# Performance work log

Hardware: AMD Instinct MI355X
Metric: run time of the kernel (lower is better)

Reference implementation:

```python
import jax, jax.numpy as jnp
import numpy as np

N_TOK = 16384   # total tokens (batch*seq)
H = 2048        # hidden_size
I = 768         # moe_intermediate_size (per-expert MLP width)
TOPK = 8        # num_experts_per_tok


def setup_inputs() -> dict:
    key = jax.random.key(0)
    ks = jax.random.split(key, 7)
    hidden_states = jax.random.normal(ks[0], (N_TOK, H), dtype=jnp.float32)
    # expert_mask[j, k] != 0 means token k selected this expert at top-k slot j
    expert_mask = jax.random.randint(ks[1], (TOPK, N_TOK), 0, 2, dtype=jnp.int32)
    routing_weights = jax.random.uniform(ks[2], (N_TOK, TOPK), dtype=jnp.float32)
    final_hidden_states = jax.random.normal(ks[3], (N_TOK, H), dtype=jnp.float32)
    gate_w = jax.random.normal(ks[4], (I, H), dtype=jnp.float32) * 0.02
    up_w = jax.random.normal(ks[5], (I, H), dtype=jnp.float32) * 0.02
    down_w = jax.random.normal(ks[6], (H, I), dtype=jnp.float32) * 0.02
    return {
        "hidden_states": hidden_states,
        "expert_mask": expert_mask,
        "routing_weights": routing_weights,
        "final_hidden_states": final_hidden_states,
        "gate_w": gate_w,
        "up_w": up_w,
        "down_w": down_w,
    }


def reference(hidden_states, expert_mask, routing_weights, final_hidden_states,
              gate_w, up_w, down_w):
    # forward_expert: gather selected tokens, SwiGLU MLP, scale by routing weight,
    # scatter-add into final_hidden_states. Equivalent jit-friendly form: the
    # combined routing weight per token is w[k] = sum_j mask[j,k]*routing_weights[k,j]
    # (tokens selected multiple times are summed, matching index_add_ semantics),
    # and unselected tokens get w[k]=0 so they contribute nothing.
    g = hidden_states @ gate_w.T                       # [N, I]
    u = hidden_states @ up_w.T                         # [N, I]
    y = (jax.nn.silu(g) * u) @ down_w.T                # [N, H]
    w = jnp.einsum('jk,kj->k', expert_mask.astype(y.dtype), routing_weights)  # [N]
    return final_hidden_states + y * w[:, None]
```

## Files before the change

kernel.cpp:

```cpp
#include <hip/hip_runtime.h>
#include <stdint.h>

#define NTOK 16384
#define HD   2048
#define ID   768
#define TOPK 8

typedef __bf16 bf16x8 __attribute__((ext_vector_type(8)));
typedef float  floatx4 __attribute__((ext_vector_type(4)));
typedef unsigned short ushort8 __attribute__((ext_vector_type(8)));

__device__ __forceinline__ unsigned short f32_to_bf16_rne(float f) {
    union { float f; uint32_t u; } v; v.f = f;
    uint32_t u = v.u;
    u += 0x7FFFu + ((u >> 16) & 1u);
    return (unsigned short)(u >> 16);
}
__device__ __forceinline__ float bf16_to_f32(unsigned short h) {
    union { uint32_t u; float f; } v; v.u = ((uint32_t)h) << 16;
    return v.f;
}

#define GLD_LDS(gsrc, ldst)                                                              \
    __builtin_amdgcn_global_load_lds(                                                    \
        (const __attribute__((address_space(1))) uint32_t*)(const void*)(gsrc),          \
        (__attribute__((address_space(3))) uint32_t*)(void*)(ldst), 16, 0, 0)

template<int VM> __device__ __forceinline__ void wait_vm() {
    if constexpr (VM == 8)      asm volatile("s_waitcnt vmcnt(8)" ::: "memory");
    else if constexpr (VM == 7) asm volatile("s_waitcnt vmcnt(7)" ::: "memory");
    else if constexpr (VM == 3) asm volatile("s_waitcnt vmcnt(3)" ::: "memory");
    else                        asm volatile("s_waitcnt vmcnt(0)" ::: "memory");
}
#define BARRIER() do { asm volatile("" ::: "memory");              \
                       __builtin_amdgcn_s_barrier();               \
                       asm volatile("" ::: "memory"); } while (0)

__global__ __launch_bounds__(256) void compute_w_kernel(const int* __restrict__ mask,
                                                        const float* __restrict__ rw,
                                                        float* __restrict__ w) {
    int k = blockIdx.x * 256 + threadIdx.x;
    if (k >= NTOK) return;
    float acc = 0.f;
#pragma unroll
    for (int j = 0; j < TOPK; ++j)
        acc += (float)mask[j * NTOK + k] * rw[k * TOPK + j];
    w[k] = acc;
}

__global__ __launch_bounds__(256) void convert_hs_kernel(const float* __restrict__ src,
                                                         unsigned short* __restrict__ dst) {
    size_t i = (size_t)blockIdx.x * 256 + threadIdx.x;
    const float4* s = (const float4*)src;
    float4 a = s[2 * i], b = s[2 * i + 1];
    ushort8 o;
    o[0] = f32_to_bf16_rne(a.x); o[1] = f32_to_bf16_rne(a.y);
    o[2] = f32_to_bf16_rne(a.z); o[3] = f32_to_bf16_rne(a.w);
    o[4] = f32_to_bf16_rne(b.x); o[5] = f32_to_bf16_rne(b.y);
    o[6] = f32_to_bf16_rne(b.z); o[7] = f32_to_bf16_rne(b.w);
    *(ushort8*)(dst + 8 * i) = o;
}

__global__ __launch_bounds__(256) void convert_w3_kernel(const float* __restrict__ g,
                                                         const float* __restrict__ u,
                                                         const float* __restrict__ d,
                                                         unsigned short* __restrict__ dst) {
    const int per = ID * HD / 8;
    int i = blockIdx.x * 256 + threadIdx.x;
    int which = i / per;
    int off = i - which * per;
    const float* src = (which == 0) ? g : ((which == 1) ? u : d);
    const float4* s = (const float4*)src;
    float4 a = s[2 * (size_t)off], b = s[2 * (size_t)off + 1];
    ushort8 o;
    o[0] = f32_to_bf16_rne(a.x); o[1] = f32_to_bf16_rne(a.y);
    o[2] = f32_to_bf16_rne(a.z); o[3] = f32_to_bf16_rne(a.w);
    o[4] = f32_to_bf16_rne(b.x); o[5] = f32_to_bf16_rne(b.y);
    o[6] = f32_to_bf16_rne(b.z); o[7] = f32_to_bf16_rne(b.w);
    *(ushort8*)(dst + 8 * (size_t)i) = o;
}

__global__ __launch_bounds__(256) void swiglu_kernel(const unsigned short* __restrict__ gu,
                                                     unsigned short* __restrict__ act) {
    int i = blockIdx.x * 256 + threadIdx.x;
    int t = i / (ID / 8);
    int c8 = i - t * (ID / 8);
    ushort8 g = *(const ushort8*)&gu[(size_t)t * (2 * ID) + c8 * 8];
    ushort8 u = *(const ushort8*)&gu[(size_t)t * (2 * ID) + ID + c8 * 8];
    ushort8 o;
#pragma unroll
    for (int j = 0; j < 8; ++j) {
        float gf = bf16_to_f32(g[j]);
        float uf = bf16_to_f32(u[j]);
        float s = gf / (1.f + __expf(-gf)) * uf;
        o[j] = f32_to_bf16_rne(s);
    }
    *(ushort8*)&act[(size_t)t * ID + c8 * 8] = o;
}

__global__ __launch_bounds__(512, 1) void gemm_gu_kernel(
    const unsigned short* __restrict__ A,
    const unsigned short* __restrict__ B,
    unsigned short* __restrict__ Cb) {
    constexpr int K = HD;
    constexpr int NT = K / 64;
    __shared__ __align__(16) unsigned char lds[2][57344];

    const int bid = blockIdx.x, nwg = gridDim.x;
    const int nb = (bid & 7) * (nwg >> 3) + (bid >> 3);
    const int bx = nb & 7, by = nb >> 3;
    const int row0 = by * 256, col0 = bx * 192;

    const int tid = threadIdx.x, wid = tid >> 6, lane = tid & 63;
    const int wr = wid >> 2, wc = wid & 3;
    const int lrow = lane & 15, q = lane >> 4;
    const int rsw = ((q ^ ((lrow >> 1) & 3)) << 4);

    const int kswz = (((lane & 3) ^ ((lane >> 3) & 3)) << 3);
    const unsigned short* sA[2];
#pragma unroll
    for (int h = 0; h < 2; ++h) {
        const int o = h * 8192 + wid * 1024 + lane * 16;
        sA[h] = A + (size_t)(row0 + (o >> 6)) * K + kswz;
    }
    const unsigned short* sB[3];
#pragma unroll
    for (int r = 0; r < 3; ++r) {
        const int o = r * 8192 + tid * 16;
        const int ks = (o >= 12288) ? 1 : 0;
        const int brow = (o - ks * 12288) >> 6;
        sB[r] = B + (size_t)(col0 + brow) * K + ks * 32 + kswz;
    }

#define STAGE_A(sb, ks, kt) do {                                                            \
        GLD_LDS(sA[0] + (kt) * 64 + (ks) * 32, lds[sb] + (ks) * 16384 + wid * 1024);        \
        GLD_LDS(sA[1] + (kt) * 64 + (ks) * 32, lds[sb] + (ks) * 16384 + 8192 + wid * 1024); \
    } while (0)
#define STAGE_B01(sb, kt) do {                                                              \
        GLD_LDS(sB[0] + (kt) * 64, lds[sb] + 32768 + wid * 1024);                           \
        GLD_LDS(sB[1] + (kt) * 64, lds[sb] + 32768 + 8192 + wid * 1024);                    \
    } while (0)
#define STAGE_B2(sb, kt)                                                                    \
        GLD_LDS(sB[2] + (kt) * 64, lds[sb] + 32768 + 16384 + wid * 1024)

#define READ_A03(s, ks) do { const unsigned char* rgn = lds[s] + (ks) * 16384;              \
        _Pragma("unroll")                                                                   \
        for (int m = 0; m < 4; ++m)                                                         \
            af[m] = *(const bf16x8*)(rgn + (wr * 128 + m * 16 + lrow) * 64 + rsw);          \
    } while (0)
#define READ_A47(s, ks) do { const unsigned char* rgn = lds[s] + (ks) * 16384;              \
        _Pragma("unroll")                                                                   \
        for (int m = 4; m < 8; ++m)                                                         \
            af[m] = *(const bf16x8*)(rgn + (wr * 128 + m * 16 + lrow) * 64 + rsw);          \
    } while (0)
#define READ_B(s, ks) do { const unsigned char* rgn = lds[s] + 32768 + (ks) * 12288;        \
        _Pragma("unroll")                                                                   \
        for (int n = 0; n < 3; ++n)                                                         \
            bb[n] = *(const bf16x8*)(rgn + (wc * 48 + n * 16 + lrow) * 64 + rsw);           \
    } while (0)
#define MFMA_H(mh) do {                                                                     \
        __builtin_amdgcn_s_setprio(1);                                                      \
        _Pragma("unroll")                                                                   \
        for (int m = (mh) * 4; m < (mh) * 4 + 4; ++m)                                       \
            _Pragma("unroll")                                                               \
            for (int n = 0; n < 3; ++n)                                                     \
                acc[m][n] = __builtin_amdgcn_mfma_f32_16x16x32_bf16(af[m], bb[n], acc[m][n], 0, 0, 0); \
        __builtin_amdgcn_s_setprio(0);                                                      \
    } while (0)

    floatx4 acc[8][3];
#pragma unroll
    for (int m = 0; m < 8; ++m)
#pragma unroll
        for (int n = 0; n < 3; ++n) acc[m][n] = (floatx4){0.f, 0.f, 0.f, 0.f};
    bf16x8 af[8], bb[3];

    STAGE_A(0, 0, 0);
    STAGE_B01(0, 0);
    STAGE_A(0, 1, 0);
    STAGE_B2(0, 0);
    wait_vm<3>();
    BARRIER();

    for (int t = 0; t < NT - 1; ++t) {
        const int s = t & 1, sn = s ^ 1;
        READ_B(s, 0); READ_A03(s, 0);
        STAGE_A(sn, 0, t + 1);
        STAGE_B01(sn, t + 1);
        MFMA_H(0);
        BARRIER();
        READ_A47(s, 0);
        STAGE_A(sn, 1, t + 1);
        STAGE_B2(sn, t + 1);
        MFMA_H(1);
        wait_vm<7>();
        BARRIER();
        READ_B(s, 1); READ_A03(s, 1);
        MFMA_H(0);
        BARRIER();
        READ_A47(s, 1);
        MFMA_H(1);
        wait_vm<3>();
        BARRIER();
    }
    {
        const int s = (NT - 1) & 1;
        READ_B(s, 0); READ_A03(s, 0);
        MFMA_H(0);
        READ_A47(s, 0);
        MFMA_H(1);
        wait_vm<0>();
        BARRIER();
        READ_B(s, 1); READ_A03(s, 1);
        MFMA_H(0);
        READ_A47(s, 1);
        MFMA_H(1);
    }
#undef STAGE_A
#undef STAGE_B01
#undef STAGE_B2
#undef READ_A03
#undef READ_A47
#undef READ_B
#undef MFMA_H

#pragma unroll
    for (int m = 0; m < 8; ++m)
#pragma unroll
        for (int r = 0; r < 4; ++r) {
            const int row = row0 + wr * 128 + m * 16 + q * 4 + r;
#pragma unroll
            for (int n = 0; n < 3; ++n) {
                const int col = col0 + wc * 48 + n * 16 + lrow;
                Cb[(size_t)row * (2 * ID) + col] = f32_to_bf16_rne(acc[m][n][r]);
            }
        }
}

__global__ __launch_bounds__(256, 2) void gemm_down_kernel(
    const unsigned short* __restrict__ A,
    const unsigned short* __restrict__ B,
    const float* __restrict__ fin,
    const float* __restrict__ wtok,
    float* __restrict__ out) {
    constexpr int K = ID;
    constexpr int NT = K / 64;
    __shared__ __align__(16) unsigned char lds[2][32768];

    const int bid = blockIdx.x, nwg = gridDim.x;
    const int nb = (bid & 7) * (nwg >> 3) + (bid >> 3);
    const int bx = nb & 15, by = nb >> 4;
    const int row0 = by * 128, col0 = bx * 128;

    const int tid = threadIdx.x, wid = tid >> 6, lane = tid & 63;
    const int wr = wid >> 1, wc = wid & 1;
    const int lrow = lane & 15, q = lane >> 4;

    const int srow = wid * 8 + (lane >> 3);
    const int sk = (((lane & 7) ^ ((lane >> 3) & 7)) << 3);
    const unsigned short* sA[4];
    const unsigned short* sB[4];
#pragma unroll
    for (int r = 0; r < 4; ++r) {
        sA[r] = A + (size_t)(row0 + r * 32 + srow) * K + sk;
        sB[r] = B + (size_t)(col0 + r * 32 + srow) * K + sk;
    }

#define STAGE_T(sb, kt) do {                                                    \
        _Pragma("unroll")                                                       \
        for (int r = 0; r < 4; ++r)                                             \
            GLD_LDS(sA[r] + (kt) * 64, lds[sb] + r * 4096 + wid * 1024);        \
        _Pragma("unroll")                                                       \
        for (int r = 0; r < 4; ++r)                                             \
            GLD_LDS(sB[r] + (kt) * 64, lds[sb] + 16384 + r * 4096 + wid * 1024);\
    } while (0)

    floatx4 acc[4][4];
#pragma unroll
    for (int m = 0; m < 4; ++m)
#pragma unroll
        for (int n = 0; n < 4; ++n) acc[m][n] = (floatx4){0.f, 0.f, 0.f, 0.f};
    bf16x8 af[4], bb[4];

    STAGE_T(0, 0);

    for (int t = 0; t < NT; ++t) {
        const int s = t & 1;
        if (t + 1 < NT) {
            STAGE_T(s ^ 1, t + 1);
            wait_vm<8>();
        } else {
            wait_vm<0>();
        }
        BARRIER();
        const unsigned char* la = lds[s];
        const unsigned char* lb = lds[s] + 16384;
#pragma unroll
        for (int ks = 0; ks < 2; ++ks) {
#pragma unroll
            for (int m = 0; m < 4; ++m)
                af[m] = *(const bf16x8*)(la + (wr * 64 + m * 16 + lrow) * 128 +
                                         (((ks * 4 + q) ^ (lrow & 7)) << 4));
#pragma unroll
            for (int n = 0; n < 4; ++n)
                bb[n] = *(const bf16x8*)(lb + (wc * 64 + n * 16 + lrow) * 128 +
                                         (((ks * 4 + q) ^ (lrow & 7)) << 4));
            __builtin_amdgcn_s_setprio(1);
#pragma unroll
            for (int m = 0; m < 4; ++m)
#pragma unroll
                for (int n = 0; n < 4; ++n)
                    acc[m][n] = __builtin_amdgcn_mfma_f32_16x16x32_bf16(af[m], bb[n], acc[m][n], 0, 0, 0);
            __builtin_amdgcn_s_setprio(0);
        }
        BARRIER();
    }
#undef STAGE_T

#pragma unroll
    for (int m = 0; m < 4; ++m)
#pragma unroll
        for (int r = 0; r < 4; ++r) {
            const int row = row0 + wr * 64 + m * 16 + q * 4 + r;
            const float wv = wtok[row];
#pragma unroll
            for (int n = 0; n < 4; ++n) {
                const int col = col0 + wc * 64 + n * 16 + lrow;
                out[(size_t)row * HD + col] = fin[(size_t)row * HD + col] + wv * acc[m][n][r];
            }
        }
}

extern "C" void kernel_launch(void* const* d_in, const int* in_sizes, int n_in,
                              void* d_out, int out_size, void* d_ws, size_t ws_size,
                              hipStream_t stream) {
    const float* hs   = (const float*)d_in[0];
    const int*   mask = (const int*)d_in[1];
    const float* rw   = (const float*)d_in[2];
    const float* fin  = (const float*)d_in[3];
    const float* gw   = (const float*)d_in[4];
    const float* uw   = (const float*)d_in[5];
    const float* dw   = (const float*)d_in[6];
    float* out = (float*)d_out;

    char* ws = (char*)d_ws;
    unsigned short* hs_b   = (unsigned short*)ws; ws += (size_t)NTOK * HD * 2;
    unsigned short* wcat_b = (unsigned short*)ws; ws += (size_t)3 * ID * HD * 2;
    unsigned short* gu_b   = (unsigned short*)ws; ws += (size_t)NTOK * 2 * ID * 2;
    float* wtok = (float*)ws;
    unsigned short* act_b = hs_b;
    unsigned short* down_b = wcat_b + (size_t)2 * ID * HD;

    compute_w_kernel<<<NTOK / 256, 256, 0, stream>>>(mask, rw, wtok);
    convert_hs_kernel<<<(NTOK * HD / 8) / 256, 256, 0, stream>>>(hs, hs_b);
    convert_w3_kernel<<<(3 * ID * HD / 8) / 256, 256, 0, stream>>>(gw, uw, dw, wcat_b);

    gemm_gu_kernel<<<512, 512, 0, stream>>>(hs_b, wcat_b, gu_b);

    swiglu_kernel<<<(NTOK * (ID / 8)) / 256, 256, 0, stream>>>(gu_b, act_b);

    gemm_down_kernel<<<2048, 256, 0, stream>>>(act_b, down_b, fin, wtok, out);
}
```

Measured before the change: 244.4 us.

## Fuse SwiGLU into gate/up GEMM epilogue via interleaved weight layout

Gate and up weight rows are interleaved in blocks of 8 during conversion, so each 16-column MFMA tile holds matching gate and up columns. The GEMM epilogue pairs them with a lane shuffle, computes SiLU(g)*u and writes the activation directly. This removes the separate SwiGLU kernel and the round trip of the full gate/up intermediate through memory. The main loop is also reordered to read all A fragments at once, with different wait counts, which raises register pressure and shifts how loads overlap with MFMAs.

```diff
diff --git a/kernel.cpp b/kernel.cpp
--- a/kernel.cpp
+++ b/kernel.cpp
@@ -28,7 +28,7 @@
 
 template<int VM> __device__ __forceinline__ void wait_vm() {
     if constexpr (VM == 8)      asm volatile("s_waitcnt vmcnt(8)" ::: "memory");
-    else if constexpr (VM == 7) asm volatile("s_waitcnt vmcnt(7)" ::: "memory");
+    else if constexpr (VM == 4) asm volatile("s_waitcnt vmcnt(4)" ::: "memory");
     else if constexpr (VM == 3) asm volatile("s_waitcnt vmcnt(3)" ::: "memory");
     else                        asm volatile("s_waitcnt vmcnt(0)" ::: "memory");
 }
@@ -65,43 +65,31 @@
                                                          const float* __restrict__ u,
                                                          const float* __restrict__ d,
                                                          unsigned short* __restrict__ dst) {
-    const int per = ID * HD / 8;
     int i = blockIdx.x * 256 + threadIdx.x;
-    int which = i / per;
-    int off = i - which * per;
-    const float* src = (which == 0) ? g : ((which == 1) ? u : d);
+    size_t e = (size_t)i * 8;
+    const float* src;
+    if (e < (size_t)2 * ID * HD) {
+        int rd = (int)(e / HD);
+        int c  = (int)(e - (size_t)rd * HD);
+        int b = rd >> 4, h = (rd >> 3) & 1, sub = rd & 7;
+        src = (h ? u : g) + (size_t)(b * 8 + sub) * HD + c;
+    } else {
+        src = d + (e - (size_t)2 * ID * HD);
+    }
     const float4* s = (const float4*)src;
-    float4 a = s[2 * (size_t)off], b = s[2 * (size_t)off + 1];
+    float4 a = s[0], bq = s[1];
     ushort8 o;
-    o[0] = f32_to_bf16_rne(a.x); o[1] = f32_to_bf16_rne(a.y);
-    o[2] = f32_to_bf16_rne(a.z); o[3] = f32_to_bf16_rne(a.w);
-    o[4] = f32_to_bf16_rne(b.x); o[5] = f32_to_bf16_rne(b.y);
-    o[6] = f32_to_bf16_rne(b.z); o[7] = f32_to_bf16_rne(b.w);
-    *(ushort8*)(dst + 8 * (size_t)i) = o;
-}
-
-__global__ __launch_bounds__(256) void swiglu_kernel(const unsigned short* __restrict__ gu,
-                                                     unsigned short* __restrict__ act) {
-    int i = blockIdx.x * 256 + threadIdx.x;
-    int t = i / (ID / 8);
-    int c8 = i - t * (ID / 8);
-    ushort8 g = *(const ushort8*)&gu[(size_t)t * (2 * ID) + c8 * 8];
-    ushort8 u = *(const ushort8*)&gu[(size_t)t * (2 * ID) + ID + c8 * 8];
-    ushort8 o;
-#pragma unroll
-    for (int j = 0; j < 8; ++j) {
-        float gf = bf16_to_f32(g[j]);
-        float uf = bf16_to_f32(u[j]);
-        float s = gf / (1.f + __expf(-gf)) * uf;
-        o[j] = f32_to_bf16_rne(s);
-    }
-    *(ushort8*)&act[(size_t)t * ID + c8 * 8] = o;
+    o[0] = f32_to_bf16_rne(a.x);  o[1] = f32_to_bf16_rne(a.y);
+    o[2] = f32_to_bf16_rne(a.z);  o[3] = f32_to_bf16_rne(a.w);
+    o[4] = f32_to_bf16_rne(bq.x); o[5] = f32_to_bf16_rne(bq.y);
+    o[6] = f32_to_bf16_rne(bq.z); o[7] = f32_to_bf16_rne(bq.w);
+    *(ushort8*)(dst + e) = o;
 }
 
 __global__ __launch_bounds__(512, 1) void gemm_gu_kernel(
     const unsigned short* __restrict__ A,
     const unsigned short* __restrict__ B,
-    unsigned short* __restrict__ Cb) {
+    unsigned short* __restrict__ act) {
     constexpr int K = HD;
     constexpr int NT = K / 64;
     __shared__ __align__(16) unsigned char lds[2][57344];
@@ -143,14 +131,9 @@
 #define STAGE_B2(sb, kt)                                                                    \
         GLD_LDS(sB[2] + (kt) * 64, lds[sb] + 32768 + 16384 + wid * 1024)
 
-#define READ_A03(s, ks) do { const unsigned char* rgn = lds[s] + (ks) * 16384;              \
+#define READ_A(s, ks) do { const unsigned char* rgn = lds[s] + (ks) * 16384;                \
         _Pragma("unroll")                                                                   \
-        for (int m = 0; m < 4; ++m)                                                         \
-            af[m] = *(const bf16x8*)(rgn + (wr * 128 + m * 16 + lrow) * 64 + rsw);          \
-    } while (0)
-#define READ_A47(s, ks) do { const unsigned char* rgn = lds[s] + (ks) * 16384;              \
-        _Pragma("unroll")                                                                   \
-        for (int m = 4; m < 8; ++m)                                                         \
+        for (int m = 0; m < 8; ++m)                                                         \
             af[m] = *(const bf16x8*)(rgn + (wr * 128 + m * 16 + lrow) * 64 + rsw);          \
     } while (0)
 #define READ_B(s, ks) do { const unsigned char* rgn = lds[s] + 32768 + (ks) * 12288;        \
@@ -184,43 +167,39 @@
 
     for (int t = 0; t < NT - 1; ++t) {
         const int s = t & 1, sn = s ^ 1;
-        READ_B(s, 0); READ_A03(s, 0);
+        READ_A(s, 0); READ_B(s, 0);
         STAGE_A(sn, 0, t + 1);
+        MFMA_H(0);
+        BARRIER();
         STAGE_B01(sn, t + 1);
+        MFMA_H(1);
+        wait_vm<4>();
+        BARRIER();
+        READ_A(s, 1); READ_B(s, 1);
+        STAGE_A(sn, 1, t + 1);
         MFMA_H(0);
         BARRIER();
-        READ_A47(s, 0);
-        STAGE_A(sn, 1, t + 1);
         STAGE_B2(sn, t + 1);
         MFMA_H(1);
-        wait_vm<7>();
-        BARRIER();
-        READ_B(s, 1); READ_A03(s, 1);
-        MFMA_H(0);
-        BARRIER();
-        READ_A47(s, 1);
-        MFMA_H(1);
         wait_vm<3>();
         BARRIER();
     }
     {
         const int s = (NT - 1) & 1;
-        READ_B(s, 0); READ_A03(s, 0);
+        READ_A(s, 0); READ_B(s, 0);
         MFMA_H(0);
-        READ_A47(s, 0);
+        BARRIER();
         MFMA_H(1);
         wait_vm<0>();
         BARRIER();
-        READ_B(s, 1); READ_A03(s, 1);
+        READ_A(s, 1); READ_B(s, 1);
         MFMA_H(0);
-        READ_A47(s, 1);
         MFMA_H(1);
     }
 #undef STAGE_A
 #undef STAGE_B01
 #undef STAGE_B2
-#undef READ_A03
-#undef READ_A47
+#undef READ_A
 #undef READ_B
 #undef MFMA_H
 
@@ -231,8 +210,14 @@
             const int row = row0 + wr * 128 + m * 16 + q * 4 + r;
 #pragma unroll
             for (int n = 0; n < 3; ++n) {
-                const int col = col0 + wc * 48 + n * 16 + lrow;
-                Cb[(size_t)row * (2 * ID) + col] = f32_to_bf16_rne(acc[m][n][r]);
+                const float v = acc[m][n][r];
+                const float p = __shfl_xor(v, 8, 64);
+                const float gf = v, uf = p;
+                const float s = gf / (1.f + __expf(-gf)) * uf;
+                if ((lrow & 8) == 0) {
+                    const int ibase = (col0 + wc * 48 + n * 16) >> 1;
+                    act[(size_t)row * ID + ibase + (lrow & 7)] = f32_to_bf16_rne(s);
+                }
             }
         }
 }
@@ -346,18 +331,15 @@
     char* ws = (char*)d_ws;
     unsigned short* hs_b   = (unsigned short*)ws; ws += (size_t)NTOK * HD * 2;
     unsigned short* wcat_b = (unsigned short*)ws; ws += (size_t)3 * ID * HD * 2;
-    unsigned short* gu_b   = (unsigned short*)ws; ws += (size_t)NTOK * 2 * ID * 2;
+    unsigned short* act_b  = (unsigned short*)ws; ws += (size_t)NTOK * ID * 2;
     float* wtok = (float*)ws;
-    unsigned short* act_b = hs_b;
     unsigned short* down_b = wcat_b + (size_t)2 * ID * HD;
 
     compute_w_kernel<<<NTOK / 256, 256, 0, stream>>>(mask, rw, wtok);
     convert_hs_kernel<<<(NTOK * HD / 8) / 256, 256, 0, stream>>>(hs, hs_b);
     convert_w3_kernel<<<(3 * ID * HD / 8) / 256, 256, 0, stream>>>(gw, uw, dw, wcat_b);
 
-    gemm_gu_kernel<<<512, 512, 0, stream>>>(hs_b, wcat_b, gu_b);
-
-    swiglu_kernel<<<(NTOK * (ID / 8)) / 256, 256, 0, stream>>>(gu_b, act_b);
+    gemm_gu_kernel<<<512, 512, 0, stream>>>(hs_b, wcat_b, act_b);
 
     gemm_down_kernel<<<2048, 256, 0, stream>>>(act_b, down_b, fin, wtok, out);
 }
```

New measurement: 233.1 us. 1.05x faster.
